# Optimization experiments

Hardware: AMD Instinct MI355X
Metric: run time of the kernel (lower is better)

Reference implementation:

```python
import jax, jax.numpy as jnp
import numpy as np

TOP_P = 0.9
B, D, H, O, E = 8192, 1024, 2048, 1024, 8


def setup_inputs() -> dict:
    key = jax.random.key(0)
    ks = jax.random.split(key, 6)
    def init(k, shape, fan_in):
        return (jax.random.normal(k, shape, jnp.float32) * (fan_in ** -0.5)).astype(jnp.float32)
    return {
        "x": jax.random.normal(ks[0], (B, D), jnp.float32),
        "gate_w": init(ks[1], (D, E), D),
        "gate_b": jnp.zeros((E,), jnp.float32),
        "w1": init(ks[2], (E, D, H), D),
        "b1": jnp.zeros((E, H), jnp.float32),
        "w2": init(ks[3], (E, H, O), H),
        "b2": jnp.zeros((E, O), jnp.float32),
    }


def reference(x, gate_w, gate_b, w1, b1, w2, b2):
    # gate + softmax
    logits = x @ gate_w + gate_b                      # [B,E]
    probs = jax.nn.softmax(logits, axis=-1)
    # all-expert MLP (batched over experts); torch GELU default is exact (erf)
    h = jax.nn.gelu(jnp.einsum('bd,edh->beh', x, w1) + b1[None], approximate=False)
    all_out = jnp.einsum('beh,eho->beo', h, w2) + b2[None]  # [B,E,O]
    # routing (entropy) loss
    routing_loss = (-jnp.sum(probs * jnp.log(probs + 1e-8), axis=-1)).mean()
    # diversity (gram logdet) loss
    mean_probs = probs.mean(axis=0)[:, None]          # [E,1]
    expert_mean = all_out.mean(axis=0)                # [E,O]
    norm = jnp.linalg.norm(expert_mean, axis=1, keepdims=True) + 1e-6
    V = mean_probs * (expert_mean / norm)             # [E,O]
    gram = V @ V.T + 1e-6 * jnp.eye(E, dtype=V.dtype)
    diversity_loss = -jnp.linalg.slogdet(gram)[1]
    # top-p mask over experts
    order = jnp.argsort(-probs, axis=-1)              # descending
    p_sorted = jnp.take_along_axis(probs, order, axis=-1)
    cum = jnp.cumsum(p_sorted, axis=-1)
    mask = cum <= TOP_P
    mask = mask.at[:, 0].set(True)
    inv = jnp.argsort(order, axis=-1)                 # inverse permutation
    mask_orig = jnp.take_along_axis(mask, inv, axis=-1)
    # normalized masked combine
    mp = probs * mask_orig.astype(probs.dtype)
    wts = mp / (mp.sum(axis=-1, keepdims=True) + 1e-8)
    output = jnp.einsum('be,beo->bo', wts, all_out)
    return output, routing_loss, diversity_loss
```

## Files before the change

kernel.cpp:

```cpp
#include <hip/hip_runtime.h>
#include <cstdint>
#include <cstddef>
#include <cmath>

#define B_ 8192
#define D_ 1024
#define H_ 2048
#define O_ 1024
#define E_ 8

typedef __bf16 bf16;
typedef __bf16 bf16x8 __attribute__((ext_vector_type(8)));
typedef __bf16 bf16x4v __attribute__((ext_vector_type(4)));
typedef float f32x4 __attribute__((ext_vector_type(4)));

typedef __attribute__((address_space(1))) void gvoid;
typedef __attribute__((address_space(3))) void lvoid;

__device__ __forceinline__ void gload16(const void* g, void* l) {
  __builtin_amdgcn_global_load_lds((gvoid*)g, (lvoid*)l, 16u, 0, 0);
}

__device__ __forceinline__ float fast_erff(float x) {
  float ax = __builtin_fabsf(x);
  float t = 1.f / (1.f + 0.3275911f * ax);
  float p = t * (0.254829592f +
            t * (-0.284496736f +
            t * (1.421413741f +
            t * (-1.453152027f +
            t * 1.061405429f))));
  float r = 1.f - p * __expf(-ax * ax);
  return __builtin_copysignf(r, x);
}
__device__ __forceinline__ float gelu_exact(float v) {
  return 0.5f * v * (1.f + fast_erff(v * 0.70710678118654752f));
}

__global__ __launch_bounds__(256) void convert_x_kernel(const float* __restrict__ x,
                                                        bf16* __restrict__ xb) {
  size_t i = (size_t)blockIdx.x * 256 + threadIdx.x;
  float4 v = ((const float4*)x)[i];
  bf16x4v o;
  o[0] = (bf16)v.x; o[1] = (bf16)v.y; o[2] = (bf16)v.z; o[3] = (bf16)v.w;
  ((bf16x4v*)xb)[i] = o;
}

__global__ __launch_bounds__(256) void transpose_w_kernel(const float* __restrict__ w,
                                                          bf16* __restrict__ wt,
                                                          int R, int C) {
  __shared__ float tile[32][33];
  int e = blockIdx.z;
  int c0 = blockIdx.x * 32, r0 = blockIdx.y * 32;
  int tx = threadIdx.x, ty = threadIdx.y;
  const float* we = w + (size_t)e * R * C;
  bf16* wte = wt + (size_t)e * R * C;
#pragma unroll
  for (int k = 0; k < 4; ++k) {
    int r = ty + 8 * k;
    tile[r][tx] = we[(size_t)(r0 + r) * C + c0 + tx];
  }
  __syncthreads();
#pragma unroll
  for (int k = 0; k < 4; ++k) {
    int c = ty + 8 * k;
    wte[(size_t)(c0 + c) * R + r0 + tx] = (bf16)tile[tx][c];
  }
}

__global__ __launch_bounds__(256) void gating_kernel(const float* __restrict__ x,
                                                     const float* __restrict__ gw,
                                                     const float* __restrict__ gb,
                                                     float* __restrict__ probs,
                                                     float* __restrict__ wts,
                                                     float* __restrict__ ent) {
  int w = threadIdx.x >> 6, l = threadIdx.x & 63;
  int b = blockIdx.x * 4 + w;
  const float* xr = x + (size_t)b * D_;
  float acc[E_];
#pragma unroll
  for (int e = 0; e < E_; ++e) acc[e] = 0.f;
  for (int j = 0; j < D_ / 64; ++j) {
    int d = j * 64 + l;
    float xv = xr[d];
    const float* g = gw + (size_t)d * E_;
#pragma unroll
    for (int e = 0; e < E_; ++e) acc[e] += xv * g[e];
  }
#pragma unroll
  for (int off = 32; off; off >>= 1)
#pragma unroll
    for (int e = 0; e < E_; ++e) acc[e] += __shfl_down(acc[e], off);

  if (l == 0) {
    float lg[E_], p[E_];
    float mx = -1e30f;
#pragma unroll
    for (int e = 0; e < E_; ++e) { lg[e] = acc[e] + gb[e]; mx = fmaxf(mx, lg[e]); }
    float s = 0.f;
#pragma unroll
    for (int e = 0; e < E_; ++e) { p[e] = expf(lg[e] - mx); s += p[e]; }
    float inv = 1.f / s;
    float en = 0.f;
#pragma unroll
    for (int e = 0; e < E_; ++e) { p[e] *= inv; en -= p[e] * logf(p[e] + 1e-8f); }
    ent[b] = en;
#pragma unroll
    for (int e = 0; e < E_; ++e) probs[(size_t)b * E_ + e] = p[e];
    int idx[E_]; float ps[E_];
#pragma unroll
    for (int e = 0; e < E_; ++e) { idx[e] = e; ps[e] = p[e]; }
    for (int i = 0; i < E_ - 1; ++i)
      for (int j = 0; j < E_ - 1 - i; ++j)
        if (ps[j] < ps[j + 1]) {
          float tp = ps[j]; ps[j] = ps[j + 1]; ps[j + 1] = tp;
          int ti = idx[j]; idx[j] = idx[j + 1]; idx[j + 1] = ti;
        }
    float cum = 0.f; float mp[E_];
#pragma unroll
    for (int e = 0; e < E_; ++e) mp[e] = 0.f;
    for (int i = 0; i < E_; ++i) {
      cum += ps[i];
      bool m = (cum <= 0.9f) || (i == 0);
      if (m) mp[idx[i]] = ps[i];
    }
    float ssum = 0.f;
#pragma unroll
    for (int e = 0; e < E_; ++e) ssum += mp[e];
    float invs = 1.f / (ssum + 1e-8f);
#pragma unroll
    for (int e = 0; e < E_; ++e) wts[(size_t)b * E_ + e] = mp[e] * invs;
  }
}

__device__ __forceinline__ void gemm_loop_gl(const bf16* __restrict__ A,
                                             const bf16* __restrict__ Bt,
                                             int K, int rowBase, int colBase,
                                             bf16* lA, bf16* lB, f32x4 acc[4][4]) {
  const int tid = threadIdx.x;
  const int w = tid >> 6, l = tid & 63;
  const int wm = w >> 1, wn = w & 1;
  const int fm = l & 15, fc = l >> 4;
  const int lr = l >> 3;
  const int pos = l & 7;
  const int gch = pos ^ lr;

  const bf16* gA = A + (size_t)(rowBase + w * 8 + lr) * K + gch * 8;
  const bf16* gB = Bt + (size_t)(colBase + w * 8 + lr) * K + gch * 8;
  bf16* dA = lA + (w * 8 + lr) * 64 + pos * 8;
  bf16* dB = lB + (w * 8 + lr) * 64 + pos * 8;

  for (int k0 = 0; k0 < K; k0 += 64) {
    __syncthreads();
#pragma unroll
    for (int j = 0; j < 4; ++j) {
      gload16(gA + (size_t)(j * 32) * K + k0, dA + j * 2048);
      gload16(gB + (size_t)(j * 32) * K + k0, dB + j * 2048);
    }
    __syncthreads();

#pragma unroll
    for (int kh = 0; kh < 2; ++kh) {
      bf16x8 af[4], bb[4];
#pragma unroll
      for (int mt = 0; mt < 4; ++mt) {
        int r = wm * 64 + mt * 16 + fm;
        int p2 = (kh * 4 + fc) ^ (r & 7);
        af[mt] = *(const bf16x8*)(lA + (size_t)r * 64 + p2 * 8);
      }
#pragma unroll
      for (int nt = 0; nt < 4; ++nt) {
        int r = wn * 64 + nt * 16 + fm;
        int p2 = (kh * 4 + fc) ^ (r & 7);
        bb[nt] = *(const bf16x8*)(lB + (size_t)r * 64 + p2 * 8);
      }
#pragma unroll
      for (int mt = 0; mt < 4; ++mt)
#pragma unroll
        for (int nt = 0; nt < 4; ++nt)
          acc[mt][nt] = __builtin_amdgcn_mfma_f32_16x16x32_bf16(af[mt], bb[nt], acc[mt][nt], 0, 0, 0);
    }
  }
}

__global__ __launch_bounds__(256, 4) void gemm1_v12_kernel(const bf16* __restrict__ xb,
                                                           const bf16* __restrict__ w1t,
                                                           const float* __restrict__ b1,
                                                           const float* __restrict__ wts,
                                                           bf16* __restrict__ h_chunk,
                                                           float* __restrict__ hsum,
                                                           int rowOffset, int Bc) {
  __shared__ bf16 smem[16384];
  bf16* lA = smem;
  bf16* lB = smem + 8192;
  f32x4 acc[4][4];
#pragma unroll
  for (int mt = 0; mt < 4; ++mt)
#pragma unroll
    for (int nt = 0; nt < 4; ++nt) acc[mt][nt] = 0.f;

  const int flat = blockIdx.y * 128 + blockIdx.x;
  const int xcd = flat & 7, lin = flat >> 3;
  const int cb = xcd * 16 + (lin & 15);
  const int rb = lin >> 4;
  const int colBase = cb * 128;
  const int rowLocal = rb * 128;
  const int rowGlobal = rowOffset + rowLocal;
  const int e = colBase >> 11;

  gemm_loop_gl(xb, w1t, D_, rowGlobal, colBase, lA, lB, acc);

  const int tid = threadIdx.x;
  const int w = tid >> 6, l = tid & 63;
  const int wm = w >> 1, wn = w & 1;
  const int fm = l & 15, fc = l >> 4;
  bf16* he = h_chunk + (size_t)e * Bc * H_;
  const int hc0 = colBase & (H_ - 1);

  float wgt[4][4];
#pragma unroll
  for (int mt = 0; mt < 4; ++mt)
#pragma unroll
    for (int i = 0; i < 4; ++i) {
      int gr = rowGlobal + wm * 64 + mt * 16 + fc * 4 + i;
      wgt[mt][i] = wts[(size_t)gr * E_ + e];
    }

  __syncthreads();
#pragma unroll
  for (int nt = 0; nt < 4; ++nt) {
    int c = wn * 64 + nt * 16 + fm;
    float bias = b1[colBase + c];
    float csum = 0.f;
#pragma unroll
    for (int mt = 0; mt < 4; ++mt) {
      int rbse = wm * 64 + mt * 16 + fc * 4;
#pragma unroll
      for (int i = 0; i < 4; ++i) {
        int r = rbse + i;
        float v = gelu_exact(acc[mt][nt][i] + bias);
        csum += v;
        smem[(size_t)r * 128 + (((c >> 3) ^ (r & 7)) << 3) + (c & 7)] = (bf16)(v * wgt[mt][i]);
      }
    }
    csum += __shfl_down(csum, 32);
    csum += __shfl_down(csum, 16);
    if (fc == 0) atomicAdd(&hsum[colBase + c], csum);
  }
  __syncthreads();

#pragma unroll
  for (int j = 0; j < 8; ++j) {
    int row = j * 16 + (tid >> 4);
    int cchunk = tid & 15;
    bf16x8 v = *(const bf16x8*)(smem + (size_t)row * 128 + (size_t)(cchunk ^ (row & 7)) * 8);
    *(bf16x8*)(he + (size_t)(rowLocal + row) * H_ + hc0 + cchunk * 8) = v;
  }
}

template <int SPLIT>
__global__ __launch_bounds__(256, 4) void gemm2_v12_kernel(const bf16* __restrict__ h_chunk,
                                                           const bf16* __restrict__ w2t,
                                                           const float* __restrict__ b2,
                                                           const float* __restrict__ wts,
                                                           float* __restrict__ out_chunk,
                                                           int rowOffset, int Bc) {
  __shared__ bf16 smem[16384];
  bf16* lA = smem;
  bf16* lB = smem + 8192;
  f32x4 acc[4][4];
#pragma unroll
  for (int mt = 0; mt < 4; ++mt)
#pragma unroll
    for (int nt = 0; nt < 4; ++nt) acc[mt][nt] = 0.f;

  const int colBase = blockIdx.x * 128;
  const int rowLocal = blockIdx.y * 128;
  const int s = blockIdx.z;
  const int g = E_ / SPLIT, e0 = s * g;

  for (int e = e0; e < e0 + g; ++e)
    gemm_loop_gl(h_chunk + (size_t)e * Bc * H_, w2t + (size_t)e * O_ * H_, H_,
                 rowLocal, colBase, lA, lB, acc);

  const int w = threadIdx.x >> 6, l = threadIdx.x & 63;
  const int wm = w >> 1, wn = w & 1;
  const int fm = l & 15, fc = l >> 4;
#pragma unroll
  for (int nt = 0; nt < 4; ++nt) {
    int gc = colBase + wn * 64 + nt * 16 + fm;
    float b2v[E_];
    if (s == 0) {
#pragma unroll
      for (int e = 0; e < E_; ++e) b2v[e] = b2[(size_t)e * O_ + gc];
    }
#pragma unroll
    for (int mt = 0; mt < 4; ++mt) {
      int lrb = rowLocal + wm * 64 + mt * 16 + fc * 4;
#pragma unroll
      for (int i = 0; i < 4; ++i) {
        int lr2 = lrb + i;
        float v = acc[mt][nt][i];
        if (s == 0) {
          const float4* wr = (const float4*)(wts + (size_t)(rowOffset + lr2) * E_);
          float4 w0 = wr[0], w1v = wr[1];
          v += w0.x * b2v[0] + w0.y * b2v[1] + w0.z * b2v[2] + w0.w * b2v[3] +
               w1v.x * b2v[4] + w1v.y * b2v[5] + w1v.z * b2v[6] + w1v.w * b2v[7];
        }
        float* op = out_chunk + (size_t)lr2 * O_ + gc;
        if (SPLIT == 1) *op = v;
        else atomicAdd(op, v);
      }
    }
  }
}

__global__ __launch_bounds__(256) void esum_kernel(const float* __restrict__ hsum,
                                                   const float* __restrict__ w2,
                                                   float* __restrict__ esum2) {
  int e = blockIdx.y;
  int o = blockIdx.x * 256 + threadIdx.x;
  const float* w2e = w2 + (size_t)e * H_ * O_;
  const float* hs = hsum + (size_t)e * H_;
  float a0 = 0.f, a1 = 0.f;
  for (int h = 0; h < H_; h += 2) {
    a0 += hs[h] * w2e[(size_t)h * O_ + o];
    a1 += hs[h + 1] * w2e[(size_t)(h + 1) * O_ + o];
  }
  esum2[(size_t)e * O_ + o] = a0 + a1;
}

__device__ __forceinline__ void gemm_loop(const bf16* __restrict__ A,
                                          const bf16* __restrict__ Bt,
                                          int K, int rowBase, int colBase,
                                          bf16* lA, bf16* lB, f32x4 acc[4][4]) {
  const int tid = threadIdx.x;
  const int w = tid >> 6, l = tid & 63;
  const int wm = w >> 1, wn = w & 1;
  const int fm = l & 15, fc = l >> 4;
  const int lr = l >> 2, lc = l & 3;
  const int sr0 = (w * 2 + 0) * 16 + lr;
  const int sr1 = (w * 2 + 1) * 16 + lr;
  const int cg0 = lc ^ ((sr0 >> 1) & 3);
  const int cg1 = lc ^ ((sr1 >> 1) & 3);
  const bf16* gA0 = A + (size_t)(rowBase + sr0) * K + cg0 * 8;
  const bf16* gA1 = A + (size_t)(rowBase + sr1) * K + cg1 * 8;
  const bf16* gB0 = Bt + (size_t)(colBase + sr0) * K + cg0 * 8;
  const bf16* gB1 = Bt + (size_t)(colBase + sr1) * K + cg1 * 8;
  bf16* lA0 = lA + (w * 2 + 0) * 512;
  bf16* lA1 = lA + (w * 2 + 1) * 512;
  bf16* lB0 = lB + (w * 2 + 0) * 512;
  bf16* lB1 = lB + (w * 2 + 1) * 512;

  for (int k0 = 0; k0 < K; k0 += 32) {
    __syncthreads();
    gload16(gA0 + k0, lA0);
    gload16(gA1 + k0, lA1);
    gload16(gB0 + k0, lB0);
    gload16(gB1 + k0, lB1);
    __syncthreads();

    bf16x8 af[4], bb[4];
#pragma unroll
    for (int mt = 0; mt < 4; ++mt) {
      int r = wm * 64 + mt * 16 + fm;
      af[mt] = *(const bf16x8*)(lA + (size_t)(r * 4 + (fc ^ ((r >> 1) & 3))) * 8);
    }
#pragma unroll
    for (int nt = 0; nt < 4; ++nt) {
      int r = wn * 64 + nt * 16 + fm;
      bb[nt] = *(const bf16x8*)(lB + (size_t)(r * 4 + (fc ^ ((r >> 1) & 3))) * 8);
    }
#pragma unroll
    for (int mt = 0; mt < 4; ++mt)
#pragma unroll
      for (int nt = 0; nt < 4; ++nt)
        acc[mt][nt] = __builtin_amdgcn_mfma_f32_16x16x32_bf16(af[mt], bb[nt], acc[mt][nt], 0, 0, 0);
  }
}

__global__ __launch_bounds__(256) void gemm1_gelu_kernel(const bf16* __restrict__ xb,
                                                         const bf16* __restrict__ w1te,
                                                         const float* __restrict__ b1e,
                                                         bf16* __restrict__ h) {
  __shared__ bf16 lA[128 * 32];
  __shared__ bf16 lB[128 * 32];
  f32x4 acc[4][4];
#pragma unroll
  for (int mt = 0; mt < 4; ++mt)
#pragma unroll
    for (int nt = 0; nt < 4; ++nt) acc[mt][nt] = 0.f;

  int rowBase = blockIdx.y * 128, colBase = blockIdx.x * 128;
  gemm_loop(xb, w1te, D_, rowBase, colBase, lA, lB, acc);

  const int w = threadIdx.x >> 6, l = threadIdx.x & 63;
  const int wm = w >> 1, wn = w & 1;
#pragma unroll
  for (int mt = 0; mt < 4; ++mt)
#pragma unroll
    for (int nt = 0; nt < 4; ++nt) {
      int gc = colBase + wn * 64 + nt * 16 + (l & 15);
      float bias = b1e[gc];
#pragma unroll
      for (int i = 0; i < 4; ++i) {
        int gr = rowBase + wm * 64 + mt * 16 + (l >> 4) * 4 + i;
        float v = gelu_exact(acc[mt][nt][i] + bias);
        h[(size_t)gr * H_ + gc] = (bf16)v;
      }
    }
}

__global__ __launch_bounds__(256) void gemm2_fused_kernel(const bf16* __restrict__ h,
                                                          const bf16* __restrict__ w2te,
                                                          const float* __restrict__ b2e,
                                                          const float* __restrict__ wts,
                                                          int e,
                                                          float* __restrict__ out,
                                                          float* __restrict__ esum) {
  __shared__ bf16 lA[128 * 32];
  __shared__ bf16 lB[128 * 32];
  f32x4 acc[4][4];
#pragma unroll
  for (int mt = 0; mt < 4; ++mt)
#pragma unroll
    for (int nt = 0; nt < 4; ++nt) acc[mt][nt] = 0.f;

  int rowBase = blockIdx.y * 128, colBase = blockIdx.x * 128;
  gemm_loop(h, w2te, H_, rowBase, colBase, lA, lB, acc);

  const int w = threadIdx.x >> 6, l = threadIdx.x & 63;
  const int wm = w >> 1, wn = w & 1;
#pragma unroll
  for (int nt = 0; nt < 4; ++nt) {
    int gc = colBase + wn * 64 + nt * 16 + (l & 15);
    float bias = b2e[gc];
    float csum = 0.f;
#pragma unroll
    for (int mt = 0; mt < 4; ++mt) {
      int grb = rowBase + wm * 64 + mt * 16 + (l >> 4) * 4;
#pragma unroll
      for (int i = 0; i < 4; ++i) {
        int gr = grb + i;
        float v = acc[mt][nt][i] + bias;
        csum += v;
        float wgt = wts[(size_t)gr * E_ + e];
        float* op = out + (size_t)gr * O_ + gc;
        *op += wgt * v;
      }
    }
    csum += __shfl_down(csum, 32);
    csum += __shfl_down(csum, 16);
    if ((l >> 4) == 0) atomicAdd(&esum[(size_t)e * O_ + gc], csum);
  }
}

template <int MODE>
__global__ __launch_bounds__(256) void scalars_kernel(const float* __restrict__ probs,
                                                      const float* __restrict__ ent,
                                                      const float* __restrict__ esum,
                                                      const float* __restrict__ b2,
                                                      float* __restrict__ outs) {
  __shared__ float red[256];
  __shared__ float Vsh[E_][O_ + 8];
  __shared__ float mp_sh[E_], norm_sh[E_];
  __shared__ float gram[E_][E_];
  int t = threadIdx.x;

  float s = 0.f;
  for (int i = t; i < B_; i += 256) s += ent[i];
  red[t] = s; __syncthreads();
  for (int off = 128; off; off >>= 1) { if (t < off) red[t] += red[t + off]; __syncthreads(); }
  if (t == 0) outs[0] = red[0] / (float)B_;
  __syncthreads();

  float mp[E_];
#pragma unroll
  for (int e = 0; e < E_; ++e) mp[e] = 0.f;
  for (int i = t; i < B_; i += 256) {
#pragma unroll
    for (int e = 0; e < E_; ++e) mp[e] += probs[(size_t)i * E_ + e];
  }
  for (int e = 0; e < E_; ++e) {
    red[t] = mp[e]; __syncthreads();
    for (int off = 128; off; off >>= 1) { if (t < off) red[t] += red[t + off]; __syncthreads(); }
    if (t == 0) mp_sh[e] = red[0] / (float)B_;
    __syncthreads();
  }

  for (int e = 0; e < E_; ++e) {
    float ss = 0.f;
    for (int o = t; o < O_; o += 256) {
      float m = esum[(size_t)e * O_ + o] / (float)B_;
      if (MODE == 1) m += b2[(size_t)e * O_ + o];
      ss += m * m;
    }
    red[t] = ss; __syncthreads();
    for (int off = 128; off; off >>= 1) { if (t < off) red[t] += red[t + off]; __syncthreads(); }
    if (t == 0) norm_sh[e] = sqrtf(red[0]) + 1e-6f;
    __syncthreads();
  }

  for (int e = 0; e < E_; ++e)
    for (int o = t; o < O_; o += 256) {
      float m = esum[(size_t)e * O_ + o] / (float)B_;
      if (MODE == 1) m += b2[(size_t)e * O_ + o];
      Vsh[e][o] = mp_sh[e] * m / norm_sh[e];
    }
  __syncthreads();

  if (t < 64) {
    int i = t >> 3, j = t & 7;
    float g = 0.f;
    for (int o = 0; o < O_; ++o) g += Vsh[i][o] * Vsh[j][o];
    if (i == j) g += 1e-6f;
    gram[i][j] = g;
  }
  __syncthreads();

  if (t == 0) {
    double a[E_][E_];
    for (int i = 0; i < E_; ++i) for (int j = 0; j < E_; ++j) a[i][j] = (double)gram[i][j];
    double ld = 0.0;
    for (int k = 0; k < E_; ++k) {
      int p = k; double mx = fabs(a[k][k]);
      for (int i = k + 1; i < E_; ++i) if (fabs(a[i][k]) > mx) { mx = fabs(a[i][k]); p = i; }
      if (p != k) for (int j = 0; j < E_; ++j) { double tmp = a[k][j]; a[k][j] = a[p][j]; a[p][j] = tmp; }
      ld += log(fabs(a[k][k]));
      double inv = 1.0 / a[k][k];
      for (int i = k + 1; i < E_; ++i) {
        double f = a[i][k] * inv;
        for (int j = k; j < E_; ++j) a[i][j] -= f * a[k][j];
      }
    }
    outs[1] = (float)(-ld);
  }
}

extern "C" void kernel_launch(void* const* d_in, const int* in_sizes, int n_in,
                              void* d_out, int out_size, void* d_ws, size_t ws_size,
                              hipStream_t stream) {
  const float* x  = (const float*)d_in[0];
  const float* gw = (const float*)d_in[1];
  const float* gb = (const float*)d_in[2];
  const float* w1 = (const float*)d_in[3];
  const float* b1 = (const float*)d_in[4];
  const float* w2 = (const float*)d_in[5];
  const float* b2 = (const float*)d_in[6];
  float* out = (float*)d_out;

  char* ws = (char*)d_ws;
  size_t need = 0;
  bf16* xb    = (bf16*)(ws + need); need += (size_t)B_ * D_ * 2;
  bf16* w1t   = (bf16*)(ws + need); need += (size_t)E_ * D_ * H_ * 2;
  bf16* w2t   = (bf16*)(ws + need); need += (size_t)E_ * H_ * O_ * 2;
  float* wts  = (float*)(ws + need); need += (size_t)B_ * E_ * 4;
  float* probs= (float*)(ws + need); need += (size_t)B_ * E_ * 4;
  float* ent  = (float*)(ws + need); need += (size_t)B_ * 4;
  float* hsum = (float*)(ws + need); need += (size_t)E_ * H_ * 4;
  float* esum = (float*)(ws + need); need += (size_t)E_ * O_ * 4;
  size_t need_common = need;
  bf16* h_chunk = (bf16*)(ws + need);

  int NC = 0;
  for (int nc = 1; nc <= 8; nc <<= 1) {
    size_t tot = need_common + (size_t)E_ * (B_ / nc) * H_ * 2;
    if (ws_size >= tot) { NC = nc; break; }
  }

  convert_x_kernel<<<(B_ * D_ / 4) / 256, 256, 0, stream>>>(x, xb);
  transpose_w_kernel<<<dim3(H_ / 32, D_ / 32, E_), dim3(32, 8), 0, stream>>>(w1, w1t, D_, H_);
  transpose_w_kernel<<<dim3(O_ / 32, H_ / 32, E_), dim3(32, 8), 0, stream>>>(w2, w2t, H_, O_);
  gating_kernel<<<B_ / 4, 256, 0, stream>>>(x, gw, gb, probs, wts, ent);

  if (NC > 0) {
    const int Bc = B_ / NC;
    const int SPLIT = (NC == 1) ? 2 : (NC == 2) ? 4 : 8;
    hipMemsetAsync(hsum, 0, (size_t)E_ * H_ * sizeof(float), stream);
    hipMemsetAsync(out, 0, (size_t)B_ * O_ * sizeof(float), stream);
    for (int c = 0; c < NC; ++c) {
      int rowOffset = c * Bc;
      gemm1_v12_kernel<<<dim3(128, Bc / 128), 256, 0, stream>>>(
          xb, w1t, b1, wts, h_chunk, hsum, rowOffset, Bc);
      float* out_chunk = out + (size_t)rowOffset * O_;
      dim3 g2(O_ / 128, Bc / 128, SPLIT);
      switch (SPLIT) {
        case 2: gemm2_v12_kernel<2><<<g2, 256, 0, stream>>>(h_chunk, w2t, b2, wts, out_chunk, rowOffset, Bc); break;
        case 4: gemm2_v12_kernel<4><<<g2, 256, 0, stream>>>(h_chunk, w2t, b2, wts, out_chunk, rowOffset, Bc); break;
        case 8: gemm2_v12_kernel<8><<<g2, 256, 0, stream>>>(h_chunk, w2t, b2, wts, out_chunk, rowOffset, Bc); break;
      }
    }
    esum_kernel<<<dim3(O_ / 256, E_), 256, 0, stream>>>(hsum, w2, esum);
    scalars_kernel<1><<<1, 256, 0, stream>>>(probs, ent, esum, b2, out + (size_t)B_ * O_);
  } else {
    bf16* he = (bf16*)(ws + need_common);
    if (ws_size < need_common + (size_t)B_ * H_ * 2) return;
    hipMemsetAsync(out, 0, (size_t)B_ * O_ * sizeof(float), stream);
    hipMemsetAsync(esum, 0, (size_t)E_ * O_ * sizeof(float), stream);
    for (int e = 0; e < E_; ++e) {
      gemm1_gelu_kernel<<<dim3(H_ / 128, B_ / 128), 256, 0, stream>>>(
          xb, w1t + (size_t)e * H_ * D_, b1 + (size_t)e * H_, he);
      gemm2_fused_kernel<<<dim3(O_ / 128, B_ / 128), 256, 0, stream>>>(
          he, w2t + (size_t)e * O_ * H_, b2 + (size_t)e * O_, wts, e, out, esum);
    }
    scalars_kernel<0><<<1, 256, 0, stream>>>(probs, ent, esum, b2, out + (size_t)B_ * O_);
  }
}
```

Baseline: 1.088 ms.

## Double-buffer LDS tiles with async global-to-LDS prefetch in GEMM loop

Replaces the single-buffered K=64 GEMM main loop with a two-stage double-buffered loop over K=32 steps. Global-to-LDS loads for step t+2 are issued while MFMAs for step t run, using explicit vmcnt waits and barriers. LDS fragment reads use inline ds_read_b128 with immediate offsets and a new 4-way XOR swizzle. This is meant to hide global load latency behind compute, but it adds barrier count per K and relies on hand-tuned waitcnt correctness.

```diff
diff --git a/kernel.cpp b/kernel.cpp
--- a/kernel.cpp
+++ b/kernel.cpp
@@ -16,9 +16,17 @@
 
 typedef __attribute__((address_space(1))) void gvoid;
 typedef __attribute__((address_space(3))) void lvoid;
+typedef __attribute__((address_space(3))) const __bf16 lbf16;
 
 __device__ __forceinline__ void gload16(const void* g, void* l) {
   __builtin_amdgcn_global_load_lds((gvoid*)g, (lvoid*)l, 16u, 0, 0);
+}
+
+template <int OFF>
+__device__ __forceinline__ bf16x8 ldsr_off(lbf16* p) {
+  float4 r;
+  asm volatile("ds_read_b128 %0, %1 offset:%2" : "=v"(r) : "v"(p), "i"(OFF));
+  return __builtin_bit_cast(bf16x8, r);
 }
 
 __device__ __forceinline__ float fast_erff(float x) {
@@ -132,57 +140,74 @@
   }
 }
 
-__device__ __forceinline__ void gemm_loop_gl(const bf16* __restrict__ A,
+__device__ __forceinline__ void gemm_loop_db(const bf16* __restrict__ A,
                                              const bf16* __restrict__ Bt,
                                              int K, int rowBase, int colBase,
-                                             bf16* lA, bf16* lB, f32x4 acc[4][4]) {
+                                             bf16* smem, f32x4 acc[4][4]) {
   const int tid = threadIdx.x;
   const int w = tid >> 6, l = tid & 63;
   const int wm = w >> 1, wn = w & 1;
   const int fm = l & 15, fc = l >> 4;
-  const int lr = l >> 3;
-  const int pos = l & 7;
-  const int gch = pos ^ lr;
-
-  const bf16* gA = A + (size_t)(rowBase + w * 8 + lr) * K + gch * 8;
-  const bf16* gB = Bt + (size_t)(colBase + w * 8 + lr) * K + gch * 8;
-  bf16* dA = lA + (w * 8 + lr) * 64 + pos * 8;
-  bf16* dB = lB + (w * 8 + lr) * 64 + pos * 8;
-
-  for (int k0 = 0; k0 < K; k0 += 64) {
-    __syncthreads();
-#pragma unroll
-    for (int j = 0; j < 4; ++j) {
-      gload16(gA + (size_t)(j * 32) * K + k0, dA + j * 2048);
-      gload16(gB + (size_t)(j * 32) * K + k0, dB + j * 2048);
-    }
-    __syncthreads();
-
-#pragma unroll
-    for (int kh = 0; kh < 2; ++kh) {
-      bf16x8 af[4], bb[4];
-#pragma unroll
-      for (int mt = 0; mt < 4; ++mt) {
-        int r = wm * 64 + mt * 16 + fm;
-        int p2 = (kh * 4 + fc) ^ (r & 7);
-        af[mt] = *(const bf16x8*)(lA + (size_t)r * 64 + p2 * 8);
-      }
-#pragma unroll
-      for (int nt = 0; nt < 4; ++nt) {
-        int r = wn * 64 + nt * 16 + fm;
-        int p2 = (kh * 4 + fc) ^ (r & 7);
-        bb[nt] = *(const bf16x8*)(lB + (size_t)r * 64 + p2 * 8);
-      }
-#pragma unroll
-      for (int mt = 0; mt < 4; ++mt)
-#pragma unroll
-        for (int nt = 0; nt < 4; ++nt)
-          acc[mt][nt] = __builtin_amdgcn_mfma_f32_16x16x32_bf16(af[mt], bb[nt], acc[mt][nt], 0, 0, 0);
-    }
-  }
-}
-
-__global__ __launch_bounds__(256, 4) void gemm1_v12_kernel(const bf16* __restrict__ xb,
+  const int pc = fc ^ (fm & 3);
+  const int srow = tid >> 2;
+  const int sch = (tid & 3) ^ (srow & 3);
+
+  const bf16* gA = A + ((size_t)rowBase + srow) * K + sch * 8;
+  const bf16* gB = Bt + ((size_t)colBase + srow) * K + sch * 8;
+  const size_t r64 = (size_t)64 * K;
+
+  bf16* dA = smem + tid * 8;
+  bf16* dB = smem + 4096 + tid * 8;
+
+#define STAGE_STEP(BUFELS, K0)                                   \
+  {                                                              \
+    gload16(gA + (K0), dA + (BUFELS));                           \
+    gload16(gA + r64 + (K0), dA + (BUFELS) + 2048);              \
+    gload16(gB + (K0), dB + (BUFELS));                           \
+    gload16(gB + r64 + (K0), dB + (BUFELS) + 2048);              \
+  }
+
+  const int nsteps = K >> 5;
+  STAGE_STEP(0, 0)
+  STAGE_STEP(8192, 32)
+  asm volatile("s_waitcnt vmcnt(4)");
+  __builtin_amdgcn_sched_barrier(0);
+  __builtin_amdgcn_s_barrier();
+
+  lbf16* pA0 = (lbf16*)smem + (wm * 64 + fm) * 32 + pc * 8;
+  lbf16* pB0 = (lbf16*)smem + 4096 + (wn * 64 + fm) * 32 + pc * 8;
+
+  for (int t = 0; t < nsteps; ++t) {
+    const int b = t & 1;
+    lbf16* pA = pA0 + b * 8192;
+    lbf16* pB = pB0 + b * 8192;
+    bf16x8 af[4], bb[4];
+    af[0] = ldsr_off<0>(pA);    af[1] = ldsr_off<1024>(pA);
+    af[2] = ldsr_off<2048>(pA); af[3] = ldsr_off<3072>(pA);
+    bb[0] = ldsr_off<0>(pB);    bb[1] = ldsr_off<1024>(pB);
+    bb[2] = ldsr_off<2048>(pB); bb[3] = ldsr_off<3072>(pB);
+    asm volatile("s_waitcnt lgkmcnt(0)");
+    __builtin_amdgcn_sched_barrier(0);
+    __builtin_amdgcn_s_barrier();
+    __builtin_amdgcn_sched_barrier(0);
+    if (t + 2 < nsteps) {
+      const int k0 = (t + 2) << 5;
+      STAGE_STEP(b * 8192, k0)
+    }
+#pragma unroll
+    for (int mt = 0; mt < 4; ++mt)
+#pragma unroll
+      for (int nt = 0; nt < 4; ++nt)
+        acc[mt][nt] = __builtin_amdgcn_mfma_f32_16x16x32_bf16(af[mt], bb[nt], acc[mt][nt], 0, 0, 0);
+    if (t + 2 < nsteps) asm volatile("s_waitcnt vmcnt(4)");
+    else                asm volatile("s_waitcnt vmcnt(0)");
+    __builtin_amdgcn_sched_barrier(0);
+    __builtin_amdgcn_s_barrier();
+  }
+#undef STAGE_STEP
+}
+
+__global__ __launch_bounds__(256, 4) void gemm1_v13_kernel(const bf16* __restrict__ xb,
                                                            const bf16* __restrict__ w1t,
                                                            const float* __restrict__ b1,
                                                            const float* __restrict__ wts,
@@ -190,8 +215,6 @@
                                                            float* __restrict__ hsum,
                                                            int rowOffset, int Bc) {
   __shared__ bf16 smem[16384];
-  bf16* lA = smem;
-  bf16* lB = smem + 8192;
   f32x4 acc[4][4];
 #pragma unroll
   for (int mt = 0; mt < 4; ++mt)
@@ -207,7 +230,7 @@
   const int rowGlobal = rowOffset + rowLocal;
   const int e = colBase >> 11;
 
-  gemm_loop_gl(xb, w1t, D_, rowGlobal, colBase, lA, lB, acc);
+  gemm_loop_db(xb, w1t, D_, rowGlobal, colBase, smem, acc);
 
   const int tid = threadIdx.x;
   const int w = tid >> 6, l = tid & 63;
@@ -258,15 +281,13 @@
 }
 
 template <int SPLIT>
-__global__ __launch_bounds__(256, 4) void gemm2_v12_kernel(const bf16* __restrict__ h_chunk,
+__global__ __launch_bounds__(256, 4) void gemm2_v13_kernel(const bf16* __restrict__ h_chunk,
                                                            const bf16* __restrict__ w2t,
                                                            const float* __restrict__ b2,
                                                            const float* __restrict__ wts,
                                                            float* __restrict__ out_chunk,
                                                            int rowOffset, int Bc) {
   __shared__ bf16 smem[16384];
-  bf16* lA = smem;
-  bf16* lB = smem + 8192;
   f32x4 acc[4][4];
 #pragma unroll
   for (int mt = 0; mt < 4; ++mt)
@@ -279,8 +300,8 @@
   const int g = E_ / SPLIT, e0 = s * g;
 
   for (int e = e0; e < e0 + g; ++e)
-    gemm_loop_gl(h_chunk + (size_t)e * Bc * H_, w2t + (size_t)e * O_ * H_, H_,
-                 rowLocal, colBase, lA, lB, acc);
+    gemm_loop_db(h_chunk + (size_t)e * Bc * H_, w2t + (size_t)e * O_ * H_, H_,
+                 rowLocal, colBase, smem, acc);
 
   const int w = threadIdx.x >> 6, l = threadIdx.x & 63;
   const int wm = w >> 1, wn = w & 1;
@@ -579,14 +600,14 @@
     hipMemsetAsync(out, 0, (size_t)B_ * O_ * sizeof(float), stream);
     for (int c = 0; c < NC; ++c) {
       int rowOffset = c * Bc;
-      gemm1_v12_kernel<<<dim3(128, Bc / 128), 256, 0, stream>>>(
+      gemm1_v13_kernel<<<dim3(128, Bc / 128), 256, 0, stream>>>(
           xb, w1t, b1, wts, h_chunk, hsum, rowOffset, Bc);
       float* out_chunk = out + (size_t)rowOffset * O_;
       dim3 g2(O_ / 128, Bc / 128, SPLIT);
       switch (SPLIT) {
-        case 2: gemm2_v12_kernel<2><<<g2, 256, 0, stream>>>(h_chunk, w2t, b2, wts, out_chunk, rowOffset, Bc); break;
-        case 4: gemm2_v12_kernel<4><<<g2, 256, 0, stream>>>(h_chunk, w2t, b2, wts, out_chunk, rowOffset, Bc); break;
-        case 8: gemm2_v12_kernel<8><<<g2, 256, 0, stream>>>(h_chunk, w2t, b2, wts, out_chunk, rowOffset, Bc); break;
+        case 2: gemm2_v13_kernel<2><<<g2, 256, 0, stream>>>(h_chunk, w2t, b2, wts, out_chunk, rowOffset, Bc); break;
+        case 4: gemm2_v13_kernel<4><<<g2, 256, 0, stream>>>(h_chunk, w2t, b2, wts, out_chunk, rowOffset, Bc); break;
+        case 8: gemm2_v13_kernel<8><<<g2, 256, 0, stream>>>(h_chunk, w2t, b2, wts, out_chunk, rowOffset, Bc); break;
       }
     }
     esum_kernel<<<dim3(O_ / 256, E_), 256, 0, stream>>>(hsum, w2, esum);
```

New measurement: 1.143 ms. +5.0%, slower.
